# Performance work log

Measured on AMD Instinct MI355X. Metric: run time of the kernel, lower is better.

The kernel has to match this reference:

```python
import jax, jax.numpy as jnp
import numpy as np

B, K, V_DIM, EMBED, HID, NTOKEN, MAX_LEN = 128, 36, 2048, 1024, 1024, 10000, 20


def _u(key, shape, scale=0.05):
    return jax.random.uniform(key, shape, jnp.float32, -scale, scale)


def setup_inputs() -> dict:
    key = jax.random.key(0)
    ks = jax.random.split(key, 12)
    d1 = HID + V_DIM + EMBED  # word_rnn input size
    d2 = V_DIM + HID          # language_rnn input size
    return dict(
        v=jax.random.normal(ks[0], (B, K, V_DIM), jnp.float32),
        caption=jax.random.normal(ks[1], (B, MAX_LEN, EMBED), jnp.float32),
        cap_len=jnp.sort(jax.random.randint(ks[2], (B,), 2, MAX_LEN + 1))[::-1].astype(jnp.int32),
        Wih1=_u(ks[3], (3 * HID, d1)), Whh1=_u(ks[4], (3 * HID, HID)),
        bih1=jnp.zeros((3 * HID,), jnp.float32), bhh1=jnp.zeros((3 * HID,), jnp.float32),
        Wih2=_u(ks[5], (3 * HID, d2)), Whh2=_u(ks[6], (3 * HID, HID)),
        bih2=jnp.zeros((3 * HID,), jnp.float32), bhh2=jnp.zeros((3 * HID,), jnp.float32),
        Wv=_u(ks[7], (HID, V_DIM)), bv=jnp.zeros((HID,), jnp.float32),
        Wq=_u(ks[8], (HID, HID)), bq=jnp.zeros((HID,), jnp.float32),
        wa=_u(ks[9], (HID,)), ba=jnp.zeros((), jnp.float32),
        W1=_u(ks[10], (HID, HID)), b1=jnp.zeros((HID,), jnp.float32),
        W2=_u(ks[11], (NTOKEN, HID)), b2=jnp.zeros((NTOKEN,), jnp.float32),
    )


def _gru(x, h, Wih, Whh, bih, bhh):
    # PyTorch GRUCell math, gate order (r, z, n)
    gi = x @ Wih.T + bih
    gh = h @ Whh.T + bhh
    ir, iz, inn = jnp.split(gi, 3, axis=-1)
    hr, hz, hn = jnp.split(gh, 3, axis=-1)
    r = jax.nn.sigmoid(ir + hr)
    z = jax.nn.sigmoid(iz + hz)
    n = jnp.tanh(inn + r * hn)
    return (1.0 - z) * n + z * h


def reference(v, caption, cap_len, Wih1, Whh1, bih1, bhh1, Wih2, Whh2, bih2, bhh2,
              Wv, bv, Wq, bq, wa, ba, W1, b1, W2, b2):
    # sort by caption length, descending (as torch forward does)
    order = jnp.argsort(-cap_len)
    v = v[order]
    caption = caption[order]
    cap_len = cap_len[order]
    v_mean = v.mean(1)                                  # [B, V_DIM]
    vproj = jax.nn.relu(v @ Wv.T + bv)                  # [B, K, HID], hoisted out of time loop

    T = MAX_LEN - 1
    dl = cap_len - 1                                    # decode lengths
    mask = (jnp.arange(T)[:, None] < dl[None, :]).astype(v.dtype)   # [T, B]
    prevs = jnp.swapaxes(caption[:, :T, :], 0, 1)       # [T, B, EMBED]

    def step(carry, xs):
        h1, h2 = carry
        prev, m = xs
        h1n = _gru(jnp.concatenate([h2, v_mean, prev], axis=1), h1, Wih1, Whh1, bih1, bhh1)
        hq = h1n @ W1.T + b1                            # h1_fcnet (dropout = identity in eval)
        # 'base' attention: softmax over objects of w^T(relu(Wv v) * relu(Wq q))
        logits = (vproj * jax.nn.relu(hq @ Wq.T + bq)[:, None, :]) @ wa + ba   # [B, K]
        att = jax.nn.softmax(logits, axis=1)
        att_v = jnp.einsum('bk,bkd->bd', att, v)        # attended image feature
        h2n = _gru(jnp.concatenate([att_v, hq], axis=1), h2, Wih2, Whh2, bih2, bhh2)
        word = h2n @ W2.T + b2                          # [B, NTOKEN]
        return (h1n, h2n), (word * m[:, None], att * m[:, None])

    init = (jnp.zeros((B, HID), v.dtype), jnp.zeros((B, HID), v.dtype))
    _, (words, atts) = jax.lax.scan(step, init, (prevs, mask))
    # pad back to max_len timesteps as the torch output buffer does
    predict = jnp.pad(jnp.swapaxes(words, 0, 1), ((0, 0), (0, 1), (0, 0)))   # [B, MAX_LEN, NTOKEN]
    alphas = jnp.pad(jnp.swapaxes(atts, 0, 1), ((0, 0), (0, 1), (0, 0)))     # [B, MAX_LEN, K]
    return predict, alphas
```

## Files before the change

### kernel.cpp

```cpp
#include <hip/hip_runtime.h>
#include <hip/hip_cooperative_groups.h>

namespace cg = cooperative_groups;

typedef unsigned short u16;
typedef __attribute__((ext_vector_type(8))) short bf16x8;
typedef __attribute__((ext_vector_type(4))) float f32x4;

#define NB 128
#define NOBJ 36
#define VDIM 2048
#define EMB 1024
#define HID 1024
#define NTOK 10000
#define MAXLEN 20
#define T_STEPS 19
#define PRED_STRIDE (MAXLEN * NTOK)
#define ALPHA_OFF ((long)NB * MAXLEN * NTOK)
#define HSZ (NB * HID)

struct Args {
  const float *v, *caption;
  const int *cap_len;
  const float *Wih1, *Whh1, *bih1, *bhh1, *Wih2, *Whh2, *bih2, *bhh2;
  const float *Wv, *bv, *Wq, *bq, *wa, *ba, *W1, *b1, *W2, *b2;
  float *out;
  int *order, *dl;
  u16 *Wvh, *vh, *Wqh, *Wql, *W1T, *Wih2c, *Wih2hql, *vproj16;
  u16 *W1aP, *W1vP, *W1cP, *Whh1P, *Whh2P, *Wih2aP, *W2P, *Wq1P, *Wih2qP;
  u16 *capphp, *capplp;
  u16 *h1hp, *h1lp, *h2hp, *h2lp, *avhp, *avlp, *vmhp, *vmlp;
  float *gv1, *gh2s, *h1f, *h2f, *gcap, *g1a, *g1c, *g2a, *g2b, *gi2h1, *qf;
  float *bq1f, *bf2f;
};

__device__ inline float b2f(u16 h) {
  unsigned u = ((unsigned)h) << 16;
  float f;
  __builtin_memcpy(&f, &u, 4);
  return f;
}
__device__ inline u16 f2b_trunc(float x) {
  unsigned u;
  __builtin_memcpy(&u, &x, 4);
  return (u16)(u >> 16);
}
__device__ inline u16 f2b_rne(float x) {
  unsigned u;
  __builtin_memcpy(&u, &x, 4);
  unsigned r = (u + 0x7fffu + ((u >> 16) & 1u)) >> 16;
  return (u16)r;
}
__device__ inline void split_bf16(float x, u16 &hi, u16 &lo) {
  hi = f2b_trunc(x);
  lo = f2b_trunc(x - b2f(hi));
}
__device__ inline bf16x8 ldb8(const u16 *p) {
  uint4 u = *(const uint4 *)p;
  bf16x8 v;
  __builtin_memcpy(&v, &u, 16);
  return v;
}
__device__ inline f32x4 mfma16(bf16x8 a, bf16x8 b, f32x4 c) {
  return __builtin_amdgcn_mfma_f32_16x16x32_bf16(a, b, c, 0, 0, 0);
}
__device__ inline float sigmoidf_(float x) {
  float e = __expf(-fabsf(x));
  float p = 1.f / (1.f + e);
  return x >= 0.f ? p : 1.f - p;
}
__device__ inline float tanhf_(float x) {
  float e = __expf(-2.f * fabsf(x));
  float t = (1.f - e) / (1.f + e);
  return x >= 0.f ? t : -t;
}
__device__ inline float wred_sum(float x) {
#pragma unroll
  for (int off = 32; off > 0; off >>= 1) x += __shfl_xor(x, off, 64);
  return x;
}
__device__ inline float wred_max(float x) {
#pragma unroll
  for (int off = 32; off > 0; off >>= 1) x = fmaxf(x, __shfl_xor(x, off, 64));
  return x;
}
__device__ inline void ntstf(float *p, float v) {
  __builtin_nontemporal_store(v, p);
}
__device__ inline f32x4 ntld4(const float *p) {
  return __builtin_nontemporal_load((const f32x4 *)p);
}

__device__ inline void cvt_hi(const float *src, u16 *dst, long n, long g0,
                              long gs) {
  for (long i = g0 * 4; i < n; i += gs * 4) {
    f32x4 f = ntld4(src + i);
    ushort4 o;
    o.x = f2b_rne(f[0]);
    o.y = f2b_rne(f[1]);
    o.z = f2b_rne(f[2]);
    o.w = f2b_rne(f[3]);
    *(ushort4 *)(dst + i) = o;
  }
}
__device__ inline void cvt_split(const float *src, u16 *dhi, u16 *dlo, long n,
                                 long g0, long gs) {
  for (long i = g0 * 4; i < n; i += gs * 4) {
    f32x4 f = ntld4(src + i);
    ushort4 h, l;
    split_bf16(f[0], h.x, l.x);
    split_bf16(f[1], h.y, l.y);
    split_bf16(f[2], h.z, l.z);
    split_bf16(f[3], h.w, l.w);
    *(ushort4 *)(dhi + i) = h;
    *(ushort4 *)(dlo + i) = l;
  }
}

__device__ inline void packW(const float *src, u16 *dst, int O, int K, int Ksrc,
                             int k0, long g0, long gs) {
  const int kblk = K >> 5;
  const long nfrag = (long)(O >> 4) * kblk * 64;
  for (long f = g0; f < nfrag; f += gs) {
    const int lane_ = (int)(f & 63);
    const long cgks = f >> 6;
    const int ks = (int)(cgks % kblk);
    const int colg = (int)(cgks / kblk);
    const int col = colg * 16 + (lane_ & 15);
    const int k = k0 + ks * 32 + (lane_ >> 4) * 8;
    const float *s = src + (long)col * Ksrc + k;
    f32x4 f0 = ntld4(s), f1 = ntld4(s + 4);
    ushort4 o0, o1;
    o0.x = f2b_rne(f0[0]);
    o0.y = f2b_rne(f0[1]);
    o0.z = f2b_rne(f0[2]);
    o0.w = f2b_rne(f0[3]);
    o1.x = f2b_rne(f1[0]);
    o1.y = f2b_rne(f1[1]);
    o1.z = f2b_rne(f1[2]);
    o1.w = f2b_rne(f1[3]);
    *(ushort4 *)(dst + f * 8) = o0;
    *(ushort4 *)(dst + f * 8 + 4) = o1;
  }
}

#define MMK_BODY                                                               \
  {                                                                            \
    const int ko = ks * 32;                                                    \
    bf16x8 va = ldb8(ah + ko);                                                 \
    bf16x8 vl;                                                                 \
    if constexpr (SPLIT) vl = ldb8(al + ko);                                   \
    _Pragma("unroll") for (int i = 0; i < NT; ++i) {                           \
      bf16x8 vb = ldb8(wr + (long)i * wstride + ko);                           \
      acc[i] = mfma16(va, vb, acc[i]);                                         \
      if constexpr (SPLIT) acc[i] = mfma16(vl, vb, acc[i]);                    \
    }                                                                          \
  }

template <int NT, bool SPLIT>
__device__ inline void mmk(f32x4 *acc, const u16 *ah, const u16 *al,
                           const u16 *wr, long wstride, int ksteps) {
#pragma unroll 2
  for (int ks = 0; ks < ksteps; ++ks) MMK_BODY
}

template <bool SPLIT>
__device__ inline f32x4 tile16(const u16 *ah, const u16 *al, const u16 *wr,
                               int K) {
  f32x4 acch = {0.f, 0.f, 0.f, 0.f};
  f32x4 accl = {0.f, 0.f, 0.f, 0.f};
  const int ksteps = K >> 5;
#pragma unroll 4
  for (int ks = 0; ks < ksteps; ++ks) {
    const int ko = ks * 32;
    bf16x8 vb = ldb8(wr + ko);
    acch = mfma16(ldb8(ah + ko), vb, acch);
    if constexpr (SPLIT) accl = mfma16(ldb8(al + ko), vb, accl);
  }
  if constexpr (SPLIT) {
#pragma unroll
    for (int r = 0; r < 4; ++r) acch[r] += accl[r];
  }
  return acch;
}

template <bool SPLIT>
__device__ inline f32x4 tile16p(const u16 *ah, const u16 *al, const u16 *bp,
                                int ksteps) {
  f32x4 acch = {0.f, 0.f, 0.f, 0.f};
  f32x4 accl = {0.f, 0.f, 0.f, 0.f};
#pragma unroll 4
  for (int ks = 0; ks < ksteps; ++ks) {
    bf16x8 vb = ldb8(bp + ks * 512);
    acch = mfma16(ldb8(ah + ks * 512), vb, acch);
    if constexpr (SPLIT) accl = mfma16(ldb8(al + ks * 512), vb, accl);
  }
  if constexpr (SPLIT) {
#pragma unroll
    for (int r = 0; r < 4; ++r) acch[r] += accl[r];
  }
  return acch;
}

__global__ void __launch_bounds__(512, 4) butd(Args a) {
  cg::grid_group grid = cg::this_grid();
  const int tid = threadIdx.x;
  const int blk = blockIdx.x;
  const int gx = gridDim.x;
  const int lane = tid & 63;
  const int wv = tid >> 6;
  const int m = lane & 15;
  const int quad = lane >> 4;
  __shared__ float sl[64];

  const long gs = (long)gx * 512;
  const long g0 = (long)blk * 512 + tid;

  packW(a.Wih1, a.W1aP, 3072, 1024, 4096, 0, g0, gs);
  packW(a.Wih1, a.W1vP, 3072, 2048, 4096, 1024, g0, gs);
  packW(a.Wih1, a.W1cP, 3072, 1024, 4096, 3072, g0, gs);
  packW(a.Whh1, a.Whh1P, 3072, 1024, 1024, 0, g0, gs);
  packW(a.Whh2, a.Whh2P, 3072, 1024, 1024, 0, g0, gs);
  packW(a.Wih2, a.Wih2aP, 3072, 2048, 3072, 0, g0, gs);
  packW(a.W2, a.W2P, NTOK, 1024, 1024, 0, g0, gs);
  cvt_hi(a.Wv, a.Wvh, 1024L * 2048, g0, gs);
  cvt_hi(a.v, a.vh, (long)NB * NOBJ * VDIM, g0, gs);
  cvt_split(a.Wq, a.Wqh, a.Wql, 1024L * 1024, g0, gs);
  for (long i = g0; i < 1024L * 1024; i += gs) {
    const int ii = (int)(i >> 10), mm2 = (int)(i & 1023);
    a.W1T[i] = f2b_rne(a.W1[(long)mm2 * 1024 + ii]);
  }
  for (long i = g0 * 4; i < 3072L * 1024; i += gs * 4) {
    const int row = (int)(i >> 10), c = (int)(i & 1023);
    f32x4 f = ntld4(a.Wih2 + (long)row * 3072 + 2048 + c);
    ushort4 h, l;
    h.x = f2b_rne(f[0]);
    h.y = f2b_rne(f[1]);
    h.z = f2b_rne(f[2]);
    h.w = f2b_rne(f[3]);
    l.x = f2b_trunc(f[0] - b2f(h.x));
    l.y = f2b_trunc(f[1] - b2f(h.y));
    l.z = f2b_trunc(f[2] - b2f(h.z));
    l.w = f2b_trunc(f[3] - b2f(h.w));
    *(ushort4 *)(a.Wih2c + i) = h;
    *(ushort4 *)(a.Wih2hql + i) = l;
  }

  if (blk == 0 && tid < NB) {
    int ki = a.cap_len[tid];
    int rank = 0;
    for (int j = 0; j < NB; ++j) {
      int kj = a.cap_len[j];
      rank += (kj > ki) || (kj == ki && j < tid);
    }
    a.order[rank] = tid;
    a.dl[rank] = ki - 1;
  }
  for (long i = g0; i < (long)NB * NTOK; i += gs) {
    long b = i / NTOK, n = i - b * NTOK;
    ntstf(&a.out[b * PRED_STRIDE + (long)(MAXLEN - 1) * NTOK + n], 0.f);
  }
  for (long i = g0; i < (long)NB * NOBJ; i += gs) {
    long b = i / NOBJ, n = i - b * NOBJ;
    ntstf(&a.out[ALPHA_OFF + b * (MAXLEN * NOBJ) + (MAXLEN - 1) * NOBJ + n],
          0.f);
  }
  for (long i = g0; i < HSZ; i += gs) {
    a.h1f[i] = 0.f;
    a.h2f[i] = 0.f;
    a.h1hp[i] = 0;
    a.h1lp[i] = 0;
    a.h2hp[i] = 0;
    a.h2lp[i] = 0;
  }
  for (long i = g0; i < 128L * 3072; i += gs) a.g1c[i] = 0.f;
  grid.sync();

  for (int b = blk; b < NB; b += gx) {
    const int ob = a.order[b];
    if (tid < 256) {
      const int d0 = tid * 8;
      const float *vb = a.v + (long)ob * NOBJ * VDIM + d0;
      float s[8] = {};
      for (int k = 0; k < NOBJ; ++k) {
        f32x4 x0 = *(const f32x4 *)(vb + (long)k * VDIM);
        f32x4 x1 = *(const f32x4 *)(vb + (long)k * VDIM + 4);
#pragma unroll
        for (int j = 0; j < 4; ++j) {
          s[j] += x0[j];
          s[4 + j] += x1[j];
        }
      }
      ushort4 H0, H1, L0, L1;
#pragma unroll
      for (int j = 0; j < 8; ++j) s[j] *= (1.f / 36.f);
      split_bf16(s[0], H0.x, L0.x);
      split_bf16(s[1], H0.y, L0.y);
      split_bf16(s[2], H0.z, L0.z);
      split_bf16(s[3], H0.w, L0.w);
      split_bf16(s[4], H1.x, L1.x);
      split_bf16(s[5], H1.y, L1.y);
      split_bf16(s[6], H1.z, L1.z);
      split_bf16(s[7], H1.w, L1.w);
      const long po = (((long)(b >> 4) * 64 + (d0 >> 5)) * 64 +
                       ((d0 >> 3) & 3) * 16 + (b & 15)) *
                      8;
      *(ushort4 *)(a.vmhp + po) = H0;
      *(ushort4 *)(a.vmhp + po + 4) = H1;
      *(ushort4 *)(a.vmlp + po) = L0;
      *(ushort4 *)(a.vmlp + po + 4) = L1;
    }
  }
  for (long f = g0; f < 19L * 8 * 32 * 64; f += gs) {
    const int lane_ = (int)(f & 63);
    long rest = f >> 6;
    const int ks = (int)(rest & 31);
    rest >>= 5;
    const int tile = (int)(rest & 7);
    const int t = (int)(rest >> 3);
    const int b = a.order[tile * 16 + (lane_ & 15)];
    const int k = ks * 32 + (lane_ >> 4) * 8;
    const float *s = a.caption + ((long)b * MAXLEN + t) * EMB + k;
    f32x4 f0 = ntld4(s), f1 = ntld4(s + 4);
    ushort4 H0, H1, L0, L1;
    split_bf16(f0[0], H0.x, L0.x);
    split_bf16(f0[1], H0.y, L0.y);
    split_bf16(f0[2], H0.z, L0.z);
    split_bf16(f0[3], H0.w, L0.w);
    split_bf16(f1[0], H1.x, L1.x);
    split_bf16(f1[1], H1.y, L1.y);
    split_bf16(f1[2], H1.z, L1.z);
    split_bf16(f1[3], H1.w, L1.w);
    *(ushort4 *)(a.capphp + f * 8) = H0;
    *(ushort4 *)(a.capphp + f * 8 + 4) = H1;
    *(ushort4 *)(a.capplp + f * 8) = L0;
    *(ushort4 *)(a.capplp + f * 8 + 4) = L1;
  }
  for (int tt = blk; tt < 576; tt += gx) {
    const int mg = tt % 36, ngr = tt / 36;
    const int row = mg * 128 + wv * 16 + m;
    const int bb = row / NOBJ, ko = row - bb * NOBJ;
    const u16 *ar = a.vh + ((long)a.order[bb] * NOBJ + ko) * VDIM + quad * 8;
    const int c0 = ngr * 64;
    const u16 *wr = a.Wvh + (long)(c0 + m) * VDIM + quad * 8;
    f32x4 acc[4] = {};
    mmk<4, false>(acc, ar, nullptr, wr, 16L * VDIM, VDIM / 32);
#pragma unroll
    for (int i = 0; i < 4; ++i) {
      const int col = c0 + i * 16 + m;
      const float bvv = a.bv[col];
#pragma unroll
      for (int r = 0; r < 4; ++r) {
        const int grow = mg * 128 + wv * 16 + quad * 4 + r;
        a.vproj16[(long)grow * HID + col] = f2b_rne(fmaxf(acc[i][r] + bvv, 0.f));
      }
    }
  }
  for (int o = blk * 8 + wv; o < 4096; o += gx * 8) {
    if (o < 1024) {
      float s = 0.f;
      for (int c = lane; c < 1024; c += 64) s += a.Wq[(long)o * 1024 + c] * a.b1[c];
      s = wred_sum(s);
      if (lane == 0) a.bq1f[o] = s + a.bq[o];
    } else {
      const int oo = o - 1024;
      float s = 0.f;
      for (int c = lane; c < 1024; c += 64)
        s += a.Wih2[(long)oo * 3072 + 2048 + c] * a.b1[c];
      s = wred_sum(s);
      if (lane == 0) a.bf2f[oo] = s;
    }
  }
  grid.sync();

  for (int task = blk; task < 5888; task += gx) {
    if (task < 192) {
      const u16 *ah = a.vmhp + (long)wv * 64 * 512 + lane * 8;
      const u16 *al = a.vmlp + (long)wv * 64 * 512 + lane * 8;
      f32x4 acc = tile16p<true>(ah, al,
                                a.W1vP + (long)task * 64 * 512 + lane * 8, 64);
      const int col = task * 16 + m;
      const float bb = a.bih1[col];
#pragma unroll
      for (int r = 0; r < 4; ++r)
        a.gv1[(long)(wv * 16 + quad * 4 + r) * 3072 + col] = acc[r] + bb;
    } else if (task < 3840) {
      const int tt2 = task - 192;
      const int tdx = tt2 / 192, ct = tt2 % 192;
      const u16 *ah = a.capphp + ((long)(tdx * 8 + wv) * 32) * 512 + lane * 8;
      const u16 *al = a.capplp + ((long)(tdx * 8 + wv) * 32) * 512 + lane * 8;
      f32x4 acc =
          tile16p<true>(ah, al, a.W1cP + (long)ct * 32 * 512 + lane * 8, 32);
      const int col = ct * 16 + m;
#pragma unroll
      for (int r = 0; r < 4; ++r)
        a.gcap[((long)tdx * NB + wv * 16 + quad * 4 + r) * 3072 + col] = acc[r];
    } else if (task < 4352) {
      const int tt2 = task - 3840;
      const int rg = tt2 >> 6, ct = tt2 & 63;
      const int row = rg * 128 + wv * 16 + m, col = ct * 16 + m;
      f32x4 acc = tile16<true>(a.Wqh + (long)row * HID + quad * 8,
                               a.Wql + (long)row * HID + quad * 8,
                               a.W1T + (long)col * HID + quad * 8, HID);
#pragma unroll
      for (int r = 0; r < 4; ++r) {
        const int n = rg * 128 + wv * 16 + quad * 4 + r;
        a.Wq1P[((long)(n >> 4) * 32 + (col >> 5)) * 512 +
               (((col >> 3) & 3) * 16 + (n & 15)) * 8 + (col & 7)] =
            f2b_rne(acc[r]);
      }
    } else {
      const int tt2 = task - 4352;
      const int rg = tt2 >> 6, ct = tt2 & 63;
      const int row = rg * 128 + wv * 16 + m, col = ct * 16 + m;
      f32x4 acc = tile16<true>(a.Wih2c + (long)row * 1024 + quad * 8,
                               a.Wih2hql + (long)row * 1024 + quad * 8,
                               a.W1T + (long)col * HID + quad * 8, HID);
#pragma unroll
      for (int r = 0; r < 4; ++r) {
        const int n = rg * 128 + wv * 16 + quad * 4 + r;
        a.Wih2qP[((long)(n >> 4) * 32 + (col >> 5)) * 512 +
                 (((col >> 3) & 3) * 16 + (n & 15)) * 8 + (col & 7)] =
            f2b_rne(acc[r]);
      }
    }
  }
  grid.sync();

  auto word_tile = [&](int wt, int tf, int pb) {
    const long ab = ((long)(pb * 8 + wv) * 32) * 512 + lane * 8;
    f32x4 acc = tile16p<true>(a.h2hp + ab, a.h2lp + ab,
                              a.W2P + (long)wt * 32 * 512 + lane * 8, 32);
    const int col = wt * 16 + m;
    const float bb = a.b2[col];
#pragma unroll
    for (int r = 0; r < 4; ++r) {
      const int grow = wv * 16 + quad * 4 + r;
      const int msk = tf < a.dl[grow];
      ntstf(&a.out[(long)grow * PRED_STRIDE + (long)tf * NTOK + col],
            msk ? acc[r] + bb : 0.f);
    }
  };

  auto attention = [&](int t, int b, int half) {
    __syncthreads();
    const int ob = a.order[b];
    const float *qrow = a.qf + (long)b * HID;
    for (int k = wv; k < NOBJ; k += 8) {
      const u16 *vp = a.vproj16 + ((long)b * NOBJ + k) * HID;
      float s = 0.f;
      for (int d = lane; d < HID; d += 64) s += b2f(vp[d]) * qrow[d] * a.wa[d];
      s = wred_sum(s);
      if (lane == 0) sl[k] = s + a.ba[0];
    }
    __syncthreads();
    if (wv == 0) {
      float x = (lane < NOBJ) ? sl[lane] : -3.0e38f;
      float mx = wred_max(x);
      float e = (lane < NOBJ) ? __expf(x - mx) : 0.f;
      float den = wred_sum(e);
      float att = e / den;
      if (lane < NOBJ) {
        sl[lane] = att;
        if (half == 0) {
          const int msk = t < a.dl[b];
          ntstf(&a.out[ALPHA_OFF + (long)b * (MAXLEN * NOBJ) + t * NOBJ + lane],
                msk ? att : 0.f);
        }
      }
    }
    __syncthreads();
    if (tid < 128) {
      const int d0 = half * 1024 + tid * 8;
      const u16 *vb = a.vh + (long)ob * NOBJ * VDIM + d0;
      float s[8] = {};
      for (int k = 0; k < NOBJ; ++k) {
        bf16x8 vv = ldb8(vb + (long)k * VDIM);
        const float w = sl[k];
#pragma unroll
        for (int j = 0; j < 8; ++j) s[j] += w * b2f((u16)vv[j]);
      }
      ushort4 H0, H1, L0, L1;
      split_bf16(s[0], H0.x, L0.x);
      split_bf16(s[1], H0.y, L0.y);
      split_bf16(s[2], H0.z, L0.z);
      split_bf16(s[3], H0.w, L0.w);
      split_bf16(s[4], H1.x, L1.x);
      split_bf16(s[5], H1.y, L1.y);
      split_bf16(s[6], H1.z, L1.z);
      split_bf16(s[7], H1.w, L1.w);
      const long po = (((long)(b >> 4) * 64 + (d0 >> 5)) * 64 +
                       ((d0 >> 3) & 3) * 16 + (b & 15)) *
                      8;
      *(ushort4 *)(a.avhp + po) = H0;
      *(ushort4 *)(a.avhp + po + 4) = H1;
      *(ushort4 *)(a.avlp + po) = L0;
      *(ushort4 *)(a.avlp + po + 4) = L1;
    }
  };

  auto S1 = [&](int t) {
    const int pr = t & 1;
    const long ab = ((long)(pr * 8 + wv) * 32) * 512 + lane * 8;
    const u16 *h2h = a.h2hp + ab;
    const u16 *h2l = a.h2lp + ab;
    for (int task = blk; task < 512; task += gx) {
      if (task < 192) {
        f32x4 acc = tile16p<true>(
            h2h, h2l, a.W1aP + (long)task * 32 * 512 + lane * 8, 32);
        const int col = task * 16 + m;
#pragma unroll
        for (int r = 0; r < 4; ++r)
          a.g1a[(long)(wv * 16 + quad * 4 + r) * 3072 + col] = acc[r];
      } else if (task < 384) {
        const int ct = task - 192;
        f32x4 acc = tile16p<true>(
            h2h, h2l, a.Whh2P + (long)ct * 32 * 512 + lane * 8, 32);
        const int col = ct * 16 + m;
        const float bb = a.bhh2[col];
#pragma unroll
        for (int r = 0; r < 4; ++r)
          a.gh2s[(long)(wv * 16 + quad * 4 + r) * 3072 + col] = acc[r] + bb;
      } else if (t > 0) {
        word_tile(task - 384, t - 1, pr);
      }
    }
  };

  auto S2 = [&](int t) {
    const int pr = t & 1, pw_ = pr ^ 1;
    const int bi = gx - 1 - blk;
    if (bi < 32) {
      const int chunk = bi * 512 + tid;
      const int row = chunk >> 7, k0 = (chunk & 127) * 8;
      const long o3 = (long)row * 3072 + k0;
      const float *gc = a.gcap + ((long)t * NB + row) * 3072 + k0;
      const long io = (long)pr * HSZ + (long)row * HID + k0;
      const long iw = (long)pw_ * HSZ + (long)row * HID + k0;
      float hn8[8];
#pragma unroll
      for (int j = 0; j < 8; ++j) {
        const int col = k0 + j;
        float ir = a.g1a[o3 + j] + gc[j] + a.gv1[o3 + j];
        float iz = a.g1a[o3 + 1024 + j] + gc[1024 + j] + a.gv1[o3 + 1024 + j];
        float in_ = a.g1a[o3 + 2048 + j] + gc[2048 + j] + a.gv1[o3 + 2048 + j];
        float hr = a.g1c[o3 + j] + a.bhh1[col];
        float hz = a.g1c[o3 + 1024 + j] + a.bhh1[HID + col];
        float hn = a.g1c[o3 + 2048 + j] + a.bhh1[2 * HID + col];
        float rr = sigmoidf_(ir + hr);
        float zz = sigmoidf_(iz + hz);
        float nn = tanhf_(in_ + rr * hn);
        hn8[j] = (1.f - zz) * nn + zz * a.h1f[io + j];
        a.h1f[iw + j] = hn8[j];
      }
      ushort4 H0, H1, L0, L1;
      split_bf16(hn8[0], H0.x, L0.x);
      split_bf16(hn8[1], H0.y, L0.y);
      split_bf16(hn8[2], H0.z, L0.z);
      split_bf16(hn8[3], H0.w, L0.w);
      split_bf16(hn8[4], H1.x, L1.x);
      split_bf16(hn8[5], H1.y, L1.y);
      split_bf16(hn8[6], H1.z, L1.z);
      split_bf16(hn8[7], H1.w, L1.w);
      const long po = (((long)(pw_ * 8 + (row >> 4)) * 32 + (k0 >> 5)) * 64 +
                       ((k0 >> 3) & 3) * 16 + (row & 15)) *
                      8;
      *(ushort4 *)(a.h1hp + po) = H0;
      *(ushort4 *)(a.h1hp + po + 4) = H1;
      *(ushort4 *)(a.h1lp + po) = L0;
      *(ushort4 *)(a.h1lp + po + 4) = L1;
    }
    if (t > 0)
      for (int task = blk; task < 320; task += gx)
        word_tile(128 + task, t - 1, pr);
  };

  auto S3 = [&](int t) {
    const int pw_ = (t & 1) ^ 1;
    const long ab = ((long)(pw_ * 8 + wv) * 32) * 512 + lane * 8;
    const u16 *h1h = a.h1hp + ab;
    const u16 *h1l = a.h1lp + ab;
    for (int task = blk; task < 381; task += gx) {
      if (task < 64) {
        f32x4 acc = tile16p<true>(
            h1h, h1l, a.Wq1P + (long)task * 32 * 512 + lane * 8, 32);
        const int col = task * 16 + m;
        const float bb = a.bq1f[col];
#pragma unroll
        for (int r = 0; r < 4; ++r)
          a.qf[(long)(wv * 16 + quad * 4 + r) * HID + col] =
              fmaxf(acc[r] + bb, 0.f);
      } else if (task < 256) {
        const int ct = task - 64;
        f32x4 acc = tile16p<true>(
            h1h, h1l, a.Wih2qP + (long)ct * 32 * 512 + lane * 8, 32);
        const int col = ct * 16 + m;
#pragma unroll
        for (int r = 0; r < 4; ++r)
          a.gi2h1[(long)(wv * 16 + quad * 4 + r) * 3072 + col] = acc[r];
      } else if (t > 0) {
        word_tile(448 + (task - 256), t - 1, t & 1);
      }
    }
  };

  auto S4 = [&](int t) {
    const int pw_ = (t & 1) ^ 1;
    for (int task = blk; task < 448; task += gx) {
      if (task < 256) {
        attention(t, task & 127, task >> 7);
      } else if (t + 1 < T_STEPS) {
        const int ct = task - 256;
        const long ab = ((long)(pw_ * 8 + wv) * 32) * 512 + lane * 8;
        f32x4 acc = tile16p<true>(a.h1hp + ab, a.h1lp + ab,
                                  a.Whh1P + (long)ct * 32 * 512 + lane * 8, 32);
        const int col = ct * 16 + m;
#pragma unroll
        for (int r = 0; r < 4; ++r)
          a.g1c[(long)(wv * 16 + quad * 4 + r) * 3072 + col] = acc[r];
      }
    }
  };

  auto S5 = [&](int t) {
    for (int task = blk; task < 436; task += gx) {
      if (task < 384) {
        const int kh = task / 192, ct = task % 192;
        const long aoff = ((long)wv * 64 + kh * 32) * 512 + lane * 8;
        f32x4 acc = tile16p<true>(
            a.avhp + aoff, a.avlp + aoff,
            a.Wih2aP + ((long)ct * 64 + kh * 32) * 512 + lane * 8, 32);
        float *dst = kh ? a.g2b : a.g2a;
        const int col = ct * 16 + m;
#pragma unroll
        for (int r = 0; r < 4; ++r)
          dst[(long)(wv * 16 + quad * 4 + r) * 3072 + col] = acc[r];
      } else if (t > 0) {
        word_tile(573 + (task - 384), t - 1, t & 1);
      }
    }
  };

  auto S6 = [&](int t) {
    const int pr = t & 1, pw_ = pr ^ 1;
    const int bi = gx - 1 - blk;
    if (bi < 32) {
      const int chunk = bi * 512 + tid;
      const int row = chunk >> 7, k0 = (chunk & 127) * 8;
      const long o3 = (long)row * 3072 + k0;
      const long io = (long)pr * HSZ + (long)row * HID + k0;
      const long iw = (long)pw_ * HSZ + (long)row * HID + k0;
      float hn8[8];
#pragma unroll
      for (int j = 0; j < 8; ++j) {
        const int col = k0 + j;
        float ir = a.g2a[o3 + j] + a.g2b[o3 + j] + a.gi2h1[o3 + j] +
                   a.bih2[col] + a.bf2f[col];
        float iz = a.g2a[o3 + 1024 + j] + a.g2b[o3 + 1024 + j] +
                   a.gi2h1[o3 + 1024 + j] + a.bih2[HID + col] +
                   a.bf2f[HID + col];
        float in_ = a.g2a[o3 + 2048 + j] + a.g2b[o3 + 2048 + j] +
                    a.gi2h1[o3 + 2048 + j] + a.bih2[2 * HID + col] +
                    a.bf2f[2 * HID + col];
        float hr = a.gh2s[o3 + j], hz = a.gh2s[o3 + 1024 + j],
              hn = a.gh2s[o3 + 2048 + j];
        float rr = sigmoidf_(ir + hr);
        float zz = sigmoidf_(iz + hz);
        float nn = tanhf_(in_ + rr * hn);
        hn8[j] = (1.f - zz) * nn + zz * a.h2f[io + j];
        a.h2f[iw + j] = hn8[j];
      }
      ushort4 H0, H1, L0, L1;
      split_bf16(hn8[0], H0.x, L0.x);
      split_bf16(hn8[1], H0.y, L0.y);
      split_bf16(hn8[2], H0.z, L0.z);
      split_bf16(hn8[3], H0.w, L0.w);
      split_bf16(hn8[4], H1.x, L1.x);
      split_bf16(hn8[5], H1.y, L1.y);
      split_bf16(hn8[6], H1.z, L1.z);
      split_bf16(hn8[7], H1.w, L1.w);
      const long po = (((long)(pw_ * 8 + (row >> 4)) * 32 + (k0 >> 5)) * 64 +
                       ((k0 >> 3) & 3) * 16 + (row & 15)) *
                      8;
      *(ushort4 *)(a.h2hp + po) = H0;
      *(ushort4 *)(a.h2hp + po + 4) = H1;
      *(ushort4 *)(a.h2lp + po) = L0;
      *(ushort4 *)(a.h2lp + po + 4) = L1;
    }
  };

  for (int t = 0; t < T_STEPS; ++t) {
    S1(t);
    grid.sync();
    S2(t);
    grid.sync();
    S3(t);
    grid.sync();
    S4(t);
    grid.sync();
    S5(t);
    grid.sync();
    S6(t);
    grid.sync();
  }
  for (int wt = blk; wt < 625; wt += gx) word_tile(wt, T_STEPS - 1, T_STEPS & 1);
}

extern "C" void kernel_launch(void *const *d_in, const int *in_sizes, int n_in,
                              void *d_out, int out_size, void *d_ws,
                              size_t ws_size, hipStream_t stream) {
  Args a;
  a.v = (const float *)d_in[0];
  a.caption = (const float *)d_in[1];
  a.cap_len = (const int *)d_in[2];
  a.Wih1 = (const float *)d_in[3];
  a.Whh1 = (const float *)d_in[4];
  a.bih1 = (const float *)d_in[5];
  a.bhh1 = (const float *)d_in[6];
  a.Wih2 = (const float *)d_in[7];
  a.Whh2 = (const float *)d_in[8];
  a.bih2 = (const float *)d_in[9];
  a.bhh2 = (const float *)d_in[10];
  a.Wv = (const float *)d_in[11];
  a.bv = (const float *)d_in[12];
  a.Wq = (const float *)d_in[13];
  a.bq = (const float *)d_in[14];
  a.wa = (const float *)d_in[15];
  a.ba = (const float *)d_in[16];
  a.W1 = (const float *)d_in[17];
  a.b1 = (const float *)d_in[18];
  a.W2 = (const float *)d_in[19];
  a.b2 = (const float *)d_in[20];
  a.out = (float *)d_out;

  char *w = (char *)d_ws;
  size_t off = 0;
  auto take = [&](size_t bytes) -> void * {
    void *p = w + off;
    off += (bytes + 255) & ~(size_t)255;
    return p;
  };
  a.order = (int *)take(NB * 4);
  a.dl = (int *)take(NB * 4);
  a.W1aP = (u16 *)take(3072UL * 1024 * 2);
  a.W1vP = (u16 *)take(3072UL * 2048 * 2);
  a.W1cP = (u16 *)take(3072UL * 1024 * 2);
  a.Whh1P = (u16 *)take(3072UL * 1024 * 2);
  a.Whh2P = (u16 *)take(3072UL * 1024 * 2);
  a.Wih2aP = (u16 *)take(3072UL * 2048 * 2);
  a.W2P = (u16 *)take((size_t)NTOK * 1024 * 2);
  a.Wq1P = (u16 *)take(1024UL * 1024 * 2);
  a.Wih2qP = (u16 *)take(3072UL * 1024 * 2);
  a.capphp = (u16 *)take(19UL * 8 * 32 * 512 * 2);
  a.capplp = (u16 *)take(19UL * 8 * 32 * 512 * 2);
  a.Wvh = (u16 *)take(1024UL * 2048 * 2);
  a.vh = (u16 *)take((size_t)NB * NOBJ * VDIM * 2);
  a.Wqh = (u16 *)take(1024UL * 1024 * 2);
  a.Wql = (u16 *)take(1024UL * 1024 * 2);
  a.W1T = (u16 *)take(1024UL * 1024 * 2);
  a.Wih2c = (u16 *)take(3072UL * 1024 * 2);
  a.Wih2hql = (u16 *)take(3072UL * 1024 * 2);
  a.vproj16 = (u16 *)take((size_t)NB * NOBJ * HID * 2);
  a.h1hp = (u16 *)take(2UL * 8 * 32 * 512 * 2);
  a.h1lp = (u16 *)take(2UL * 8 * 32 * 512 * 2);
  a.h2hp = (u16 *)take(2UL * 8 * 32 * 512 * 2);
  a.h2lp = (u16 *)take(2UL * 8 * 32 * 512 * 2);
  a.avhp = (u16 *)take(8UL * 64 * 512 * 2);
  a.avlp = (u16 *)take(8UL * 64 * 512 * 2);
  a.vmhp = (u16 *)take(8UL * 64 * 512 * 2);
  a.vmlp = (u16 *)take(8UL * 64 * 512 * 2);
  a.gv1 = (float *)take((size_t)NB * 3072 * 4);
  a.gh2s = (float *)take((size_t)NB * 3072 * 4);
  a.h1f = (float *)take((size_t)2 * HSZ * 4);
  a.h2f = (float *)take((size_t)2 * HSZ * 4);
  a.qf = (float *)take((size_t)HSZ * 4);
  a.gcap = (float *)take((size_t)T_STEPS * NB * 3072 * 4);
  a.g1a = (float *)take((size_t)NB * 3072 * 4);
  a.g1c = (float *)take((size_t)NB * 3072 * 4);
  a.g2a = (float *)take((size_t)NB * 3072 * 4);
  a.g2b = (float *)take((size_t)NB * 3072 * 4);
  a.gi2h1 = (float *)take((size_t)NB * 3072 * 4);
  a.bq1f = (float *)take(1024UL * 4);
  a.bf2f = (float *)take(3072UL * 4);

  static int gridBlocks = 0;
  if (gridBlocks == 0) {
    int occ = 0;
    if (hipOccupancyMaxActiveBlocksPerMultiprocessor(&occ, (const void *)butd,
                                                     512, 0) != hipSuccess ||
        occ < 1)
      occ = 1;
    gridBlocks = (occ >= 2) ? 512 : 256;
  }

  void *kargs[] = {(void *)&a};
  hipLaunchCooperativeKernel((const void *)butd, dim3(gridBlocks), dim3(512),
                             kargs, 0, stream);
}
```

Baseline: 9.022 ms.

## Fuse GRU gate math into gate GEMMs, cut per-step barriers, custom grid barrier

The GRU1 and GRU2 elementwise updates now run inside the epilogues of the W1a and Wih2a GEMMs. Each of these tasks computes the r, z and n column tiles together with a new three-accumulator tile routine. This removes the separate S2/S6 stages, two grid barriers per timestep and the g1a/g2a/g2b intermediate buffers. The cooperative-groups grid.sync is replaced with a hand-written flag barrier (per-block slots polled by block 0, then a generation word), and the barrier area is reset with a memset before launch. The trade-off is fewer, heavier GEMM tasks (64 instead of 192) on the critical path, scattered 2-byte stores of the packed hidden state, and a barrier whose correctness depends on the memory fences used.

```diff
diff --git a/kernel.cpp b/kernel.cpp
--- a/kernel.cpp
+++ b/kernel.cpp
@@ -1,7 +1,4 @@
 #include <hip/hip_runtime.h>
-#include <hip/hip_cooperative_groups.h>
-
-namespace cg = cooperative_groups;
 
 typedef unsigned short u16;
 typedef __attribute__((ext_vector_type(8))) short bf16x8;
@@ -18,6 +15,8 @@
 #define PRED_STRIDE (MAXLEN * NTOK)
 #define ALPHA_OFF ((long)NB * MAXLEN * NTOK)
 #define HSZ (NB * HID)
+#define BAR_GEN (512 * 16)
+#define BAR_BYTES ((512 * 16 + 16) * 4)
 
 struct Args {
   const float *v, *caption;
@@ -25,12 +24,13 @@
   const float *Wih1, *Whh1, *bih1, *bhh1, *Wih2, *Whh2, *bih2, *bhh2;
   const float *Wv, *bv, *Wq, *bq, *wa, *ba, *W1, *b1, *W2, *b2;
   float *out;
+  unsigned *bar;
   int *order, *dl;
   u16 *Wvh, *vh, *Wqh, *Wql, *W1T, *Wih2c, *Wih2hql, *vproj16;
   u16 *W1aP, *W1vP, *W1cP, *Whh1P, *Whh2P, *Wih2aP, *W2P, *Wq1P, *Wih2qP;
   u16 *capphp, *capplp;
   u16 *h1hp, *h1lp, *h2hp, *h2lp, *avhp, *avlp, *vmhp, *vmlp;
-  float *gv1, *gh2s, *h1f, *h2f, *gcap, *g1a, *g1c, *g2a, *g2b, *gi2h1, *qf;
+  float *gv1, *gh2s, *h1f, *h2f, *gcap, *g1c, *gi2h1, *qf;
   float *bq1f, *bf2f;
 };
 
@@ -89,6 +89,33 @@
 }
 __device__ inline f32x4 ntld4(const float *p) {
   return __builtin_nontemporal_load((const f32x4 *)p);
+}
+
+__device__ inline void gbar(unsigned *bar, int blk, int gx, unsigned target) {
+  __syncthreads();
+  __threadfence();
+  if (threadIdx.x == 0)
+    __hip_atomic_store(&bar[blk * 16], target, __ATOMIC_RELAXED,
+                       __HIP_MEMORY_SCOPE_AGENT);
+  if (blk == 0) {
+    for (int s = threadIdx.x; s < gx; s += 512) {
+      while (__hip_atomic_load(&bar[s * 16], __ATOMIC_RELAXED,
+                               __HIP_MEMORY_SCOPE_AGENT) < target)
+        __builtin_amdgcn_s_sleep(2);
+    }
+    __syncthreads();
+    if (threadIdx.x == 0) {
+      __threadfence();
+      __hip_atomic_store(&bar[BAR_GEN], target, __ATOMIC_RELAXED,
+                         __HIP_MEMORY_SCOPE_AGENT);
+    }
+  } else if (threadIdx.x == 0) {
+    while (__hip_atomic_load(&bar[BAR_GEN], __ATOMIC_RELAXED,
+                             __HIP_MEMORY_SCOPE_AGENT) < target)
+      __builtin_amdgcn_s_sleep(2);
+  }
+  __syncthreads();
+  __threadfence();
 }
 
 __device__ inline void cvt_hi(const float *src, u16 *dst, long n, long g0,
@@ -202,8 +229,26 @@
   return acch;
 }
 
+template <int KSTEPS>
+__device__ inline void tile3(f32x4 acc[3], const u16 *ah, const u16 *al,
+                             const u16 *b0, const u16 *b1, const u16 *b2) {
+#pragma unroll 2
+  for (int ks = 0; ks < KSTEPS; ++ks) {
+    bf16x8 va = ldb8(ah + ks * 512);
+    bf16x8 vl = ldb8(al + ks * 512);
+    bf16x8 w0 = ldb8(b0 + ks * 512);
+    bf16x8 w1 = ldb8(b1 + ks * 512);
+    bf16x8 w2 = ldb8(b2 + ks * 512);
+    acc[0] = mfma16(va, w0, acc[0]);
+    acc[1] = mfma16(va, w1, acc[1]);
+    acc[2] = mfma16(va, w2, acc[2]);
+    acc[0] = mfma16(vl, w0, acc[0]);
+    acc[1] = mfma16(vl, w1, acc[1]);
+    acc[2] = mfma16(vl, w2, acc[2]);
+  }
+}
+
 __global__ void __launch_bounds__(512, 4) butd(Args a) {
-  cg::grid_group grid = cg::this_grid();
   const int tid = threadIdx.x;
   const int blk = blockIdx.x;
   const int gx = gridDim.x;
@@ -215,6 +260,8 @@
 
   const long gs = (long)gx * 512;
   const long g0 = (long)blk * 512 + tid;
+  unsigned bgen = 1;
+  auto GB = [&]() { gbar(a.bar, blk, gx, bgen++); };
 
   packW(a.Wih1, a.W1aP, 3072, 1024, 4096, 0, g0, gs);
   packW(a.Wih1, a.W1vP, 3072, 2048, 4096, 1024, g0, gs);
@@ -274,7 +321,7 @@
     a.h2lp[i] = 0;
   }
   for (long i = g0; i < 128L * 3072; i += gs) a.g1c[i] = 0.f;
-  grid.sync();
+  GB();
 
   for (int b = blk; b < NB; b += gx) {
     const int ob = a.order[b];
@@ -291,9 +338,9 @@
           s[4 + j] += x1[j];
         }
       }
+#pragma unroll
+      for (int j = 0; j < 8; ++j) s[j] *= (1.f / 36.f);
       ushort4 H0, H1, L0, L1;
-#pragma unroll
-      for (int j = 0; j < 8; ++j) s[j] *= (1.f / 36.f);
       split_bf16(s[0], H0.x, L0.x);
       split_bf16(s[1], H0.y, L0.y);
       split_bf16(s[2], H0.z, L0.z);
@@ -371,7 +418,7 @@
       if (lane == 0) a.bf2f[oo] = s;
     }
   }
-  grid.sync();
+  GB();
 
   for (int task = blk; task < 5888; task += gx) {
     if (task < 192) {
@@ -425,7 +472,7 @@
       }
     }
   }
-  grid.sync();
+  GB();
 
   auto word_tile = [&](int wt, int tf, int pb) {
     const long ab = ((long)(pb * 8 + wv) * 32) * 512 + lane * 8;
@@ -499,209 +546,166 @@
     }
   };
 
-  auto S1 = [&](int t) {
-    const int pr = t & 1;
-    const long ab = ((long)(pr * 8 + wv) * 32) * 512 + lane * 8;
-    const u16 *h2h = a.h2hp + ab;
-    const u16 *h2l = a.h2lp + ab;
-    for (int task = blk; task < 512; task += gx) {
-      if (task < 192) {
-        f32x4 acc = tile16p<true>(
-            h2h, h2l, a.W1aP + (long)task * 32 * 512 + lane * 8, 32);
-        const int col = task * 16 + m;
-#pragma unroll
-        for (int r = 0; r < 4; ++r)
-          a.g1a[(long)(wv * 16 + quad * 4 + r) * 3072 + col] = acc[r];
-      } else if (task < 384) {
-        const int ct = task - 192;
-        f32x4 acc = tile16p<true>(
-            h2h, h2l, a.Whh2P + (long)ct * 32 * 512 + lane * 8, 32);
-        const int col = ct * 16 + m;
-        const float bb = a.bhh2[col];
-#pragma unroll
-        for (int r = 0; r < 4; ++r)
-          a.gh2s[(long)(wv * 16 + quad * 4 + r) * 3072 + col] = acc[r] + bb;
-      } else if (t > 0) {
-        word_tile(task - 384, t - 1, pr);
-      }
-    }
-  };
-
-  auto S2 = [&](int t) {
-    const int pr = t & 1, pw_ = pr ^ 1;
-    const int bi = gx - 1 - blk;
-    if (bi < 32) {
-      const int chunk = bi * 512 + tid;
-      const int row = chunk >> 7, k0 = (chunk & 127) * 8;
-      const long o3 = (long)row * 3072 + k0;
-      const float *gc = a.gcap + ((long)t * NB + row) * 3072 + k0;
-      const long io = (long)pr * HSZ + (long)row * HID + k0;
-      const long iw = (long)pw_ * HSZ + (long)row * HID + k0;
-      float hn8[8];
-#pragma unroll
-      for (int j = 0; j < 8; ++j) {
-        const int col = k0 + j;
-        float ir = a.g1a[o3 + j] + gc[j] + a.gv1[o3 + j];
-        float iz = a.g1a[o3 + 1024 + j] + gc[1024 + j] + a.gv1[o3 + 1024 + j];
-        float in_ = a.g1a[o3 + 2048 + j] + gc[2048 + j] + a.gv1[o3 + 2048 + j];
-        float hr = a.g1c[o3 + j] + a.bhh1[col];
-        float hz = a.g1c[o3 + 1024 + j] + a.bhh1[HID + col];
-        float hn = a.g1c[o3 + 2048 + j] + a.bhh1[2 * HID + col];
-        float rr = sigmoidf_(ir + hr);
-        float zz = sigmoidf_(iz + hz);
-        float nn = tanhf_(in_ + rr * hn);
-        hn8[j] = (1.f - zz) * nn + zz * a.h1f[io + j];
-        a.h1f[iw + j] = hn8[j];
-      }
-      ushort4 H0, H1, L0, L1;
-      split_bf16(hn8[0], H0.x, L0.x);
-      split_bf16(hn8[1], H0.y, L0.y);
-      split_bf16(hn8[2], H0.z, L0.z);
-      split_bf16(hn8[3], H0.w, L0.w);
-      split_bf16(hn8[4], H1.x, L1.x);
-      split_bf16(hn8[5], H1.y, L1.y);
-      split_bf16(hn8[6], H1.z, L1.z);
-      split_bf16(hn8[7], H1.w, L1.w);
-      const long po = (((long)(pw_ * 8 + (row >> 4)) * 32 + (k0 >> 5)) * 64 +
-                       ((k0 >> 3) & 3) * 16 + (row & 15)) *
-                      8;
-      *(ushort4 *)(a.h1hp + po) = H0;
-      *(ushort4 *)(a.h1hp + po + 4) = H1;
-      *(ushort4 *)(a.h1lp + po) = L0;
-      *(ushort4 *)(a.h1lp + po + 4) = L1;
-    }
-    if (t > 0)
-      for (int task = blk; task < 320; task += gx)
-        word_tile(128 + task, t - 1, pr);
-  };
-
-  auto S3 = [&](int t) {
-    const int pw_ = (t & 1) ^ 1;
-    const long ab = ((long)(pw_ * 8 + wv) * 32) * 512 + lane * 8;
-    const u16 *h1h = a.h1hp + ab;
-    const u16 *h1l = a.h1lp + ab;
-    for (int task = blk; task < 381; task += gx) {
-      if (task < 64) {
-        f32x4 acc = tile16p<true>(
-            h1h, h1l, a.Wq1P + (long)task * 32 * 512 + lane * 8, 32);
-        const int col = task * 16 + m;
-        const float bb = a.bq1f[col];
-#pragma unroll
-        for (int r = 0; r < 4; ++r)
-          a.qf[(long)(wv * 16 + quad * 4 + r) * HID + col] =
-              fmaxf(acc[r] + bb, 0.f);
-      } else if (task < 256) {
-        const int ct = task - 64;
-        f32x4 acc = tile16p<true>(
-            h1h, h1l, a.Wih2qP + (long)ct * 32 * 512 + lane * 8, 32);
-        const int col = ct * 16 + m;
-#pragma unroll
-        for (int r = 0; r < 4; ++r)
-          a.gi2h1[(long)(wv * 16 + quad * 4 + r) * 3072 + col] = acc[r];
-      } else if (t > 0) {
-        word_tile(448 + (task - 256), t - 1, t & 1);
-      }
-    }
-  };
-
-  auto S4 = [&](int t) {
-    const int pw_ = (t & 1) ^ 1;
-    for (int task = blk; task < 448; task += gx) {
-      if (task < 256) {
-        attention(t, task & 127, task >> 7);
-      } else if (t + 1 < T_STEPS) {
-        const int ct = task - 256;
-        const long ab = ((long)(pw_ * 8 + wv) * 32) * 512 + lane * 8;
-        f32x4 acc = tile16p<true>(a.h1hp + ab, a.h1lp + ab,
-                                  a.Whh1P + (long)ct * 32 * 512 + lane * 8, 32);
-        const int col = ct * 16 + m;
-#pragma unroll
-        for (int r = 0; r < 4; ++r)
-          a.g1c[(long)(wv * 16 + quad * 4 + r) * 3072 + col] = acc[r];
-      }
-    }
-  };
-
-  auto S5 = [&](int t) {
-    for (int task = blk; task < 436; task += gx) {
-      if (task < 384) {
-        const int kh = task / 192, ct = task % 192;
-        const long aoff = ((long)wv * 64 + kh * 32) * 512 + lane * 8;
-        f32x4 acc = tile16p<true>(
-            a.avhp + aoff, a.avlp + aoff,
-            a.Wih2aP + ((long)ct * 64 + kh * 32) * 512 + lane * 8, 32);
-        float *dst = kh ? a.g2b : a.g2a;
-        const int col = ct * 16 + m;
-#pragma unroll
-        for (int r = 0; r < 4; ++r)
-          dst[(long)(wv * 16 + quad * 4 + r) * 3072 + col] = acc[r];
-      } else if (t > 0) {
-        word_tile(573 + (task - 384), t - 1, t & 1);
-      }
-    }
-  };
-
-  auto S6 = [&](int t) {
-    const int pr = t & 1, pw_ = pr ^ 1;
-    const int bi = gx - 1 - blk;
-    if (bi < 32) {
-      const int chunk = bi * 512 + tid;
-      const int row = chunk >> 7, k0 = (chunk & 127) * 8;
-      const long o3 = (long)row * 3072 + k0;
-      const long io = (long)pr * HSZ + (long)row * HID + k0;
-      const long iw = (long)pw_ * HSZ + (long)row * HID + k0;
-      float hn8[8];
-#pragma unroll
-      for (int j = 0; j < 8; ++j) {
-        const int col = k0 + j;
-        float ir = a.g2a[o3 + j] + a.g2b[o3 + j] + a.gi2h1[o3 + j] +
-                   a.bih2[col] + a.bf2f[col];
-        float iz = a.g2a[o3 + 1024 + j] + a.g2b[o3 + 1024 + j] +
-                   a.gi2h1[o3 + 1024 + j] + a.bih2[HID + col] +
-                   a.bf2f[HID + col];
-        float in_ = a.g2a[o3 + 2048 + j] + a.g2b[o3 + 2048 + j] +
-                    a.gi2h1[o3 + 2048 + j] + a.bih2[2 * HID + col] +
-                    a.bf2f[2 * HID + col];
-        float hr = a.gh2s[o3 + j], hz = a.gh2s[o3 + 1024 + j],
-              hn = a.gh2s[o3 + 2048 + j];
-        float rr = sigmoidf_(ir + hr);
-        float zz = sigmoidf_(iz + hz);
-        float nn = tanhf_(in_ + rr * hn);
-        hn8[j] = (1.f - zz) * nn + zz * a.h2f[io + j];
-        a.h2f[iw + j] = hn8[j];
-      }
-      ushort4 H0, H1, L0, L1;
-      split_bf16(hn8[0], H0.x, L0.x);
-      split_bf16(hn8[1], H0.y, L0.y);
-      split_bf16(hn8[2], H0.z, L0.z);
-      split_bf16(hn8[3], H0.w, L0.w);
-      split_bf16(hn8[4], H1.x, L1.x);
-      split_bf16(hn8[5], H1.y, L1.y);
-      split_bf16(hn8[6], H1.z, L1.z);
-      split_bf16(hn8[7], H1.w, L1.w);
-      const long po = (((long)(pw_ * 8 + (row >> 4)) * 32 + (k0 >> 5)) * 64 +
-                       ((k0 >> 3) & 3) * 16 + (row & 15)) *
-                      8;
-      *(ushort4 *)(a.h2hp + po) = H0;
-      *(ushort4 *)(a.h2hp + po + 4) = H1;
-      *(ushort4 *)(a.h2lp + po) = L0;
-      *(ushort4 *)(a.h2lp + po + 4) = L1;
-    }
-  };
-
   for (int t = 0; t < T_STEPS; ++t) {
-    S1(t);
-    grid.sync();
-    S2(t);
-    grid.sync();
-    S3(t);
-    grid.sync();
-    S4(t);
-    grid.sync();
-    S5(t);
-    grid.sync();
-    S6(t);
-    grid.sync();
+    const int pr = t & 1, pw = pr ^ 1;
+
+    {
+      const long ab = ((long)(pr * 8 + wv) * 32) * 512 + lane * 8;
+      const u16 *h2h = a.h2hp + ab;
+      const u16 *h2l = a.h2lp + ab;
+      for (int task = blk; task < 456; task += gx) {
+        if (task < 64) {
+          const int cg2 = task;
+          f32x4 acc[3] = {{0.f, 0.f, 0.f, 0.f},
+                          {0.f, 0.f, 0.f, 0.f},
+                          {0.f, 0.f, 0.f, 0.f}};
+          tile3<32>(acc, h2h, h2l,
+                    a.W1aP + (long)cg2 * 32 * 512 + lane * 8,
+                    a.W1aP + (long)(64 + cg2) * 32 * 512 + lane * 8,
+                    a.W1aP + (long)(128 + cg2) * 32 * 512 + lane * 8);
+          const int col = cg2 * 16 + m;
+#pragma unroll
+          for (int r = 0; r < 4; ++r) {
+            const int row = wv * 16 + quad * 4 + r;
+            const long o3 = (long)row * 3072 + col;
+            const float *gc = a.gcap + ((long)t * NB + row) * 3072 + col;
+            float ir = acc[0][r] + a.gv1[o3] + gc[0];
+            float iz = acc[1][r] + a.gv1[o3 + 1024] + gc[1024];
+            float in_ = acc[2][r] + a.gv1[o3 + 2048] + gc[2048];
+            float hr = a.g1c[o3] + a.bhh1[col];
+            float hz = a.g1c[o3 + 1024] + a.bhh1[1024 + col];
+            float hn = a.g1c[o3 + 2048] + a.bhh1[2048 + col];
+            float rr = sigmoidf_(ir + hr);
+            float zz = sigmoidf_(iz + hz);
+            float nn = tanhf_(in_ + rr * hn);
+            const long hoff = (long)row * HID + col;
+            float hnew = (1.f - zz) * nn + zz * a.h1f[(long)pr * HSZ + hoff];
+            a.h1f[(long)pw * HSZ + hoff] = hnew;
+            u16 hi, lo;
+            split_bf16(hnew, hi, lo);
+            const long po = (((long)(pw * 8 + (row >> 4)) * 32 + (col >> 5)) *
+                                 64 +
+                             ((col >> 3) & 3) * 16 + (row & 15)) *
+                                8 +
+                            (col & 7);
+            a.h1hp[po] = hi;
+            a.h1lp[po] = lo;
+          }
+        } else if (task < 256) {
+          const int ct = task - 64;
+          f32x4 acc = tile16p<true>(
+              h2h, h2l, a.Whh2P + (long)ct * 32 * 512 + lane * 8, 32);
+          const int col = ct * 16 + m;
+          const float bb = a.bhh2[col];
+#pragma unroll
+          for (int r = 0; r < 4; ++r)
+            a.gh2s[(long)(wv * 16 + quad * 4 + r) * 3072 + col] = acc[r] + bb;
+        } else if (t > 0) {
+          word_tile(task - 256, t - 1, pr);
+        }
+      }
+    }
+    GB();
+
+    {
+      const long ab = ((long)(pw * 8 + wv) * 32) * 512 + lane * 8;
+      const u16 *h1h = a.h1hp + ab;
+      const u16 *h1l = a.h1lp + ab;
+      for (int task = blk; task < 384; task += gx) {
+        if (task < 64) {
+          f32x4 acc = tile16p<true>(
+              h1h, h1l, a.Wq1P + (long)task * 32 * 512 + lane * 8, 32);
+          const int col = task * 16 + m;
+          const float bb = a.bq1f[col];
+#pragma unroll
+          for (int r = 0; r < 4; ++r)
+            a.qf[(long)(wv * 16 + quad * 4 + r) * HID + col] =
+                fmaxf(acc[r] + bb, 0.f);
+        } else if (task < 256) {
+          const int ct = task - 64;
+          f32x4 acc = tile16p<true>(
+              h1h, h1l, a.Wih2qP + (long)ct * 32 * 512 + lane * 8, 32);
+          const int col = ct * 16 + m;
+#pragma unroll
+          for (int r = 0; r < 4; ++r)
+            a.gi2h1[(long)(wv * 16 + quad * 4 + r) * 3072 + col] = acc[r];
+        } else if (t > 0) {
+          word_tile(200 + (task - 256), t - 1, pr);
+        }
+      }
+    }
+    GB();
+
+    {
+      for (int task = blk; task < 512; task += gx) {
+        if (task < 256) {
+          attention(t, task & 127, task >> 7);
+        } else if (task < 448) {
+          if (t + 1 < T_STEPS) {
+            const int ct = task - 256;
+            const long ab = ((long)(pw * 8 + wv) * 32) * 512 + lane * 8;
+            f32x4 acc = tile16p<true>(
+                a.h1hp + ab, a.h1lp + ab,
+                a.Whh1P + (long)ct * 32 * 512 + lane * 8, 32);
+            const int col = ct * 16 + m;
+#pragma unroll
+            for (int r = 0; r < 4; ++r)
+              a.g1c[(long)(wv * 16 + quad * 4 + r) * 3072 + col] = acc[r];
+          }
+        } else if (t > 0) {
+          word_tile(328 + (task - 448), t - 1, pr);
+        }
+      }
+    }
+    GB();
+
+    {
+      for (int task = blk; task < 297; task += gx) {
+        if (task < 64) {
+          const int cg2 = task;
+          const long aoff = ((long)wv * 64) * 512 + lane * 8;
+          f32x4 acc[3] = {{0.f, 0.f, 0.f, 0.f},
+                          {0.f, 0.f, 0.f, 0.f},
+                          {0.f, 0.f, 0.f, 0.f}};
+          tile3<64>(acc, a.avhp + aoff, a.avlp + aoff,
+                    a.Wih2aP + (long)cg2 * 64 * 512 + lane * 8,
+                    a.Wih2aP + (long)(64 + cg2) * 64 * 512 + lane * 8,
+                    a.Wih2aP + (long)(128 + cg2) * 64 * 512 + lane * 8);
+          const int col = cg2 * 16 + m;
+#pragma unroll
+          for (int r = 0; r < 4; ++r) {
+            const int row = wv * 16 + quad * 4 + r;
+            const long o3 = (long)row * 3072 + col;
+            float ir = acc[0][r] + a.gi2h1[o3] + a.bih2[col] + a.bf2f[col];
+            float iz = acc[1][r] + a.gi2h1[o3 + 1024] + a.bih2[1024 + col] +
+                       a.bf2f[1024 + col];
+            float in_ = acc[2][r] + a.gi2h1[o3 + 2048] + a.bih2[2048 + col] +
+                        a.bf2f[2048 + col];
+            float hr = a.gh2s[o3];
+            float hz = a.gh2s[o3 + 1024];
+            float hn = a.gh2s[o3 + 2048];
+            float rr = sigmoidf_(ir + hr);
+            float zz = sigmoidf_(iz + hz);
+            float nn = tanhf_(in_ + rr * hn);
+            const long hoff = (long)row * HID + col;
+            float hnew = (1.f - zz) * nn + zz * a.h2f[(long)pr * HSZ + hoff];
+            a.h2f[(long)pw * HSZ + hoff] = hnew;
+            u16 hi, lo;
+            split_bf16(hnew, hi, lo);
+            const long po = (((long)(pw * 8 + (row >> 4)) * 32 + (col >> 5)) *
+                                 64 +
+                             ((col >> 3) & 3) * 16 + (row & 15)) *
+                                8 +
+                            (col & 7);
+            a.h2hp[po] = hi;
+            a.h2lp[po] = lo;
+          }
+        } else if (t > 0) {
+          word_tile(392 + (task - 64), t - 1, pr);
+        }
+      }
+    }
+    GB();
   }
   for (int wt = blk; wt < 625; wt += gx) word_tile(wt, T_STEPS - 1, T_STEPS & 1);
 }
@@ -740,6 +744,7 @@
     off += (bytes + 255) & ~(size_t)255;
     return p;
   };
+  a.bar = (unsigned *)take(BAR_BYTES);
   a.order = (int *)take(NB * 4);
   a.dl = (int *)take(NB * 4);
   a.W1aP = (u16 *)take(3072UL * 1024 * 2);
@@ -775,10 +780,7 @@
   a.h2f = (float *)take((size_t)2 * HSZ * 4);
   a.qf = (float *)take((size_t)HSZ * 4);
   a.gcap = (float *)take((size_t)T_STEPS * NB * 3072 * 4);
-  a.g1a = (float *)take((size_t)NB * 3072 * 4);
   a.g1c = (float *)take((size_t)NB * 3072 * 4);
-  a.g2a = (float *)take((size_t)NB * 3072 * 4);
-  a.g2b = (float *)take((size_t)NB * 3072 * 4);
   a.gi2h1 = (float *)take((size_t)NB * 3072 * 4);
   a.bq1f = (float *)take(1024UL * 4);
   a.bf2f = (float *)take(3072UL * 4);
@@ -793,6 +795,7 @@
     gridBlocks = (occ >= 2) ? 512 : 256;
   }
 
+  (void)hipMemsetAsync((void *)a.bar, 0, BAR_BYTES, stream);
   void *kargs[] = {(void *)&a};
   hipLaunchCooperativeKernel((const void *)butd, dim3(gridBlocks), dim3(512),
                              kargs, 0, stream);
```

Measured after the change: 9.300 ms. 1.03x slower.
